# Kernel tuning notes

Hardware: AMD Instinct MI355X
Metric: run time of the kernel (lower is better)

## Reference

```python
import jax, jax.numpy as jnp
import numpy as np

B, N, D, C, H = 8, 2048, 768, 2048, 3072
ROPE_BASE = 10000.0


def rms_norm(x, scale, eps=1e-6):
    x32 = x.astype(jnp.float32)
    normed = x32 * jax.lax.rsqrt(jnp.mean(x32 * x32, axis=-1, keepdims=True) + eps)
    return normed.astype(x.dtype) * scale


def apply_rope(x, pos):
    # x: [..., T, D], pos: [..., T] int. Half-split (llama-style) rotary embedding.
    half = x.shape[-1] // 2
    inv_freq = 1.0 / (ROPE_BASE ** (jnp.arange(half, dtype=jnp.float32) / half))
    ang = pos.astype(jnp.float32)[..., None] * inv_freq  # [..., T, half]
    cos, sin = jnp.cos(ang), jnp.sin(ang)
    x1, x2 = x[..., :half], x[..., half:]
    return jnp.concatenate([x1 * cos - x2 * sin, x1 * sin + x2 * cos], axis=-1)


def setup_inputs() -> dict:
    key = jax.random.key(0)
    ks = jax.random.split(key, 12)
    inp = {
        "latents": jax.random.normal(ks[0], (B, N, D), dtype=jnp.float32),
        "tau": jnp.float32(1.0),
        "residual_scaling": jnp.float32(1.0),
        "gumbel_noise_scale": jnp.float32(0.5),
        "positions": jnp.sort(jax.random.randint(ks[1], (B, max(N, C)), 0, 2048), axis=-1),
        # learned parameters (torch Linear weights stored [out, in])
        "codebook": jax.random.normal(ks[2], (C, D), dtype=jnp.float32),
        "norm_context_scale": jnp.ones((D,), jnp.float32),
        "norm_queries_scale": jnp.ones((D,), jnp.float32),
        "norm_ff_scale": jnp.ones((D,), jnp.float32),
        "Wq": jax.random.normal(ks[3], (D, D), jnp.float32) / np.sqrt(D),
        "Wk": jax.random.normal(ks[4], (D, D), jnp.float32) / np.sqrt(D),
        "Wv": jax.random.normal(ks[5], (D, D), jnp.float32) / np.sqrt(D),
        "bv": jnp.zeros((D,), jnp.float32),
        "Wc": jax.random.normal(ks[6], (D, D), jnp.float32) / np.sqrt(D),
        "W1": jax.random.normal(ks[7], (H, D), jnp.float32) / np.sqrt(D),
        "W2": jax.random.normal(ks[8], (D, H), jnp.float32) / np.sqrt(H),
        "W3": jax.random.normal(ks[9], (H, D), jnp.float32) / np.sqrt(D),
    }
    return inp


def reference(latents, tau, residual_scaling, gumbel_noise_scale, positions,
              codebook, norm_context_scale, norm_queries_scale, norm_ff_scale,
              Wq, Wk, Wv, bv, Wc, W1, W2, W3):
    scale = jnp.sqrt(jnp.float32(D))
    normed_context = rms_norm(codebook, norm_context_scale)        # [C, D]
    normed_queries = rms_norm(latents, norm_queries_scale)         # [B, N, D]

    q = jnp.einsum('bnd,ed->bne', normed_queries, Wq)              # [B, N, D]
    k = normed_context @ Wk.T                                      # [C, D]
    v = normed_context @ Wv.T + bv                                 # [C, D]

    q = apply_rope(q, positions[:, :N])                            # [B, N, D]
    k = apply_rope(jnp.broadcast_to(k, (B, C, D)), positions[:, :C])  # [B, C, D]

    log_alpha = jnp.einsum('bnd,bcd->bnc', q, k) / scale           # [B, N, C]

    u = jax.random.uniform(jax.random.key(42), log_alpha.shape, dtype=jnp.float32)
    gumbel = -jnp.log(-jnp.log(u + 1e-10) + 1e-10)
    log_alpha_tau = (log_alpha + gumbel_noise_scale * gumbel) / tau
    z = jax.nn.softmax(log_alpha_tau, axis=-1)                     # [B, N, C]

    attn = jnp.einsum('bnc,cd->bnd', z, v)                         # [B, N, D]
    y = jnp.einsum('bnd,ed->bne', attn, Wc)
    attn_output = residual_scaling * latents + y

    h = rms_norm(attn_output, norm_ff_scale)
    ff = jnp.einsum('bnh,dh->bnd', jax.nn.silu(jnp.einsum('bnd,hd->bnh', h, W1)) * jnp.einsum('bnd,hd->bnh', h, W3), W2)
    codebook_output = attn_output + ff
    return (codebook_output, log_alpha, log_alpha_tau, z)
```

## Files before the change

kernel.cpp:

```cpp
#include <hip/hip_runtime.h>
#include <cstdint>
#include <cstddef>


typedef __bf16 bf16_t;
typedef __bf16 bf16x8 __attribute__((ext_vector_type(8)));
typedef float  f32x4  __attribute__((ext_vector_type(4)));
typedef float  f32x16 __attribute__((ext_vector_type(16)));

#define B_    8
#define N_    2048
#define D_    768
#define C_    2048
#define H_    3072
#define NROWS 16384

#define WQ_OFF 0
#define WK_OFF 589824
#define WV_OFF 1179648
#define WC_OFF 1769472
#define W1_OFF 2359296
#define W3_OFF 4718592
#define W2_OFF 7077888
#define WTOT   9437184

#define WS_W     0ull
#define WS_TRIG  18874368ull
#define WS_VCT   25165824ull
#define WS_NC    28311552ull
#define WS_NQ    31457280ull
#define WS_Z     56623104ull
#define WS_H     28311552ull
#define WS_G     157286400ull
#define WS_VB    257949696ull

#define DO_CB    0ull
#define DO_LA    50331648ull
#define DO_LAT   184549376ull
#define DO_Z     318767104ull
#define DO_QBASE 184549376ull
#define DO_KBASE (184549376ull + 50331648ull)
#define DO_QROPE (234881024ull + 6291456ull)
#define DO_KROPE (241172480ull + 25165824ull)

__device__ __forceinline__ void gl_lds16(const void* g, void* l) {
  __builtin_amdgcn_global_load_lds((__attribute__((address_space(1))) void*)(g),
                                   (__attribute__((address_space(3))) void*)(l),
                                   16, 0, 0);
}

__device__ __forceinline__ void block_sync() {
  __builtin_amdgcn_sched_barrier(0);
  asm volatile("" ::: "memory");
  __builtin_amdgcn_s_barrier();
  asm volatile("" ::: "memory");
  __builtin_amdgcn_sched_barrier(0);
}

__device__ __forceinline__ uint32_t rotl32(uint32_t v, int d) {
  return (v << d) | (v >> (32 - d));
}
__device__ __forceinline__ void tf_round(uint32_t& x0, uint32_t& x1, int r) {
  x0 += x1; x1 = rotl32(x1, r); x1 ^= x0;
}
__device__ __forceinline__ uint2 threefry2x32(uint32_t k0, uint32_t k1,
                                              uint32_t x0, uint32_t x1) {
  const uint32_t k2 = k0 ^ k1 ^ 0x1BD11BDAu;
  x0 += k0; x1 += k1;
  tf_round(x0,x1,13); tf_round(x0,x1,15); tf_round(x0,x1,26); tf_round(x0,x1,6);
  x0 += k1; x1 += k2 + 1u;
  tf_round(x0,x1,17); tf_round(x0,x1,29); tf_round(x0,x1,16); tf_round(x0,x1,24);
  x0 += k2; x1 += k0 + 2u;
  tf_round(x0,x1,13); tf_round(x0,x1,15); tf_round(x0,x1,26); tf_round(x0,x1,6);
  x0 += k0; x1 += k1 + 3u;
  tf_round(x0,x1,17); tf_round(x0,x1,29); tf_round(x0,x1,16); tf_round(x0,x1,24);
  x0 += k1; x1 += k2 + 4u;
  tf_round(x0,x1,13); tf_round(x0,x1,15); tf_round(x0,x1,26); tf_round(x0,x1,6);
  x0 += k2; x1 += k0 + 5u;
  return make_uint2(x0, x1);
}

#define SWZ(o) ((o) ^ ((((o) >> 7) & 3) << 4))

#define PHASE_MFMA_OPEN() do { \
    block_sync(); \
    asm volatile("s_waitcnt lgkmcnt(0)" ::: "memory"); \
    __builtin_amdgcn_sched_barrier(0); \
    __builtin_amdgcn_s_setprio(1); \
  } while (0)
#define PHASE_MFMA_CLOSE() do { \
    __builtin_amdgcn_s_setprio(0); \
    __builtin_amdgcn_sched_barrier(0); \
  } while (0)

#define ROWMAP32(rg, kg) (((rg) & 3) + 8 * ((rg) >> 2) + 4 * (kg))

template <int EPI>
__global__ __launch_bounds__(512, 2) void gemm8p(
    const bf16_t* __restrict__ A, const bf16_t* __restrict__ B,
    void* outp, const void* auxp, const float* sptr,
    int M, int N, int K, long sA, long sB, long sO)
{
  __shared__ bf16_t As[2][2][8192];
  __shared__ bf16_t Bs[2][2][8192];
  const int tid  = threadIdx.x;
  const int lane = tid & 63;
  const int wid  = tid >> 6;
  const int wm = wid >> 2, wn = wid & 3;
  const int l31 = lane & 31, kg = lane >> 5;

  const int lin = (blockIdx.z * gridDim.y + blockIdx.y) * gridDim.x + blockIdx.x;
  const int swzb = (lin & 7) * 64 + (lin >> 3);
  const int bz = swzb >> 6;
  const int ny = (swzb & 63) >> 3;
  const int nx = swzb & 7;

  const bf16_t* Ab = A + (size_t)bz * (size_t)sA;
  const bf16_t* Bb = B + (size_t)bz * (size_t)sB;
  const int tm = ny * 256;
  const int tn = nx * 256;
  const int nt = K >> 6;

  const bf16_t *srcA0, *srcA1, *srcB0, *srcB1;
  {
    const int d0 = wid * 1024 + lane * 16;
    const int p0 = SWZ(d0);
    srcA0 = Ab + (size_t)(tm + (p0 >> 6)) * K + ((p0 & 63) >> 1);
    srcB0 = Bb + (size_t)(tn + (p0 >> 6)) * K + ((p0 & 63) >> 1);
    const int d1 = 8192 + wid * 1024 + lane * 16;
    const int p1 = SWZ(d1);
    srcA1 = Ab + (size_t)(tm + (p1 >> 6)) * K + ((p1 & 63) >> 1);
    srcB1 = Bb + (size_t)(tn + (p1 >> 6)) * K + ((p1 & 63) >> 1);
  }
  bf16_t* dstA = &As[0][0][0] + wid * 512;
  bf16_t* dstB = &Bs[0][0][0] + wid * 512;

  int olA[4][2], olB[2][2];
  #pragma unroll
  for (int mb = 0; mb < 4; ++mb)
    #pragma unroll
    for (int u = 0; u < 2; ++u) {
      const int o = ((wm * 128 + mb * 32 + l31) << 6) + u * 32 + (kg << 4);
      olA[mb][u] = SWZ(o);
    }
  #pragma unroll
  for (int nb = 0; nb < 2; ++nb)
    #pragma unroll
    for (int u = 0; u < 2; ++u) {
      const int o = ((wn * 64 + nb * 32 + l31) << 6) + u * 32 + (kg << 4);
      olB[nb][u] = SWZ(o);
    }

#define STG_A(tile_, kk_) do { \
    const size_t ko_ = (size_t)(tile_) * 64 + (size_t)(kk_) * 32; \
    bf16_t* db_ = dstA + (((tile_) & 1) ? 16384 : 0) + ((kk_) ? 8192 : 0); \
    gl_lds16(srcA0 + ko_, db_); \
    gl_lds16(srcA1 + ko_, db_ + 4096); \
  } while (0)
#define STG_B(tile_, kk_) do { \
    const size_t ko_ = (size_t)(tile_) * 64 + (size_t)(kk_) * 32; \
    bf16_t* db_ = dstB + (((tile_) & 1) ? 16384 : 0) + ((kk_) ? 8192 : 0); \
    gl_lds16(srcB0 + ko_, db_); \
    gl_lds16(srcB1 + ko_, db_ + 4096); \
  } while (0)

  f32x16 acc[4][2] = {};

  STG_A(0, 0); STG_B(0, 0); STG_A(0, 1); STG_B(0, 1);
  STG_B(1, 0); STG_A(1, 0); STG_B(1, 1);
  asm volatile("s_waitcnt vmcnt(6)" ::: "memory");
  block_sync();

  for (int t = 0; t < nt; ++t) {
    const int s = t & 1;
    bf16x8 bfr[2][2];
    #pragma unroll
    for (int q = 0; q < 4; ++q) {
      const int kk = q >> 1, mh = q & 1;
      if (q == 0)      { if (t + 1 < nt) STG_A(t + 1, 1); }
      else if (q == 1) { if (t + 2 < nt) STG_B(t + 2, 0); }
      else if (q == 2) { if (t + 2 < nt) STG_A(t + 2, 0); }
      else             { if (t + 2 < nt) STG_B(t + 2, 1); }
      if (mh == 0) {
        const char* Bbase = (const char*)&Bs[s][kk][0];
        #pragma unroll
        for (int nb = 0; nb < 2; ++nb)
          #pragma unroll
          for (int u = 0; u < 2; ++u)
            bfr[nb][u] = *(const bf16x8*)(Bbase + olB[nb][u]);
      }
      const char* Abase = (const char*)&As[s][kk][0];
      bf16x8 af[2][2];
      #pragma unroll
      for (int j = 0; j < 2; ++j)
        #pragma unroll
        for (int u = 0; u < 2; ++u)
          af[j][u] = *(const bf16x8*)(Abase + olA[mh * 2 + j][u]);
      PHASE_MFMA_OPEN();
      #pragma unroll
      for (int u = 0; u < 2; ++u)
        #pragma unroll
        for (int j = 0; j < 2; ++j)
          #pragma unroll
          for (int nb = 0; nb < 2; ++nb)
            acc[mh * 2 + j][nb] =
              __builtin_amdgcn_mfma_f32_32x32x16_bf16(af[j][u], bfr[nb][u], acc[mh * 2 + j][nb], 0, 0, 0);
      PHASE_MFMA_CLOSE();
      if (q == 3) asm volatile("s_waitcnt vmcnt(6)" ::: "memory");
      block_sync();
    }
  }
#undef STG_A
#undef STG_B

  #pragma unroll
  for (int mb = 0; mb < 4; ++mb) {
    #pragma unroll
    for (int nb = 0; nb < 2; ++nb) {
      const int cg = tn + wn * 64 + nb * 32 + l31;
      #pragma unroll
      for (int rg = 0; rg < 16; ++rg) {
        const int r = tm + wm * 128 + mb * 32 + ROWMAP32(rg, kg);
        const float v = acc[mb][nb][rg];
        const size_t idx = (size_t)r * N + cg;
        if (EPI == 1) {
          ((float*)outp)[(size_t)bz * sO + idx] = v * 0.03608439182435161f;
        } else {
          ((float*)outp)[(size_t)bz * sO + idx] = v;
        }
      }
    }
  }
}

template <int EPI>
__global__ __launch_bounds__(512, 2) void gemm_n384(
    const bf16_t* __restrict__ A, const bf16_t* __restrict__ B,
    void* outp, const void* auxp, const float* sptr, int K)
{
  __shared__ bf16_t As[2][2][4096];
  __shared__ bf16_t Bs[2][2][12288];
  const int tid  = threadIdx.x;
  const int lane = tid & 63;
  const int wid  = tid >> 6;
  const int wm = wid >> 2, wn = wid & 3;
  const int l31 = lane & 31, kg = lane >> 5;

  const int lin = blockIdx.y * 2 + blockIdx.x;
  const int swzb = (lin & 7) * 32 + (lin >> 3);
  const int ny = swzb >> 1;
  const int nx = swzb & 1;

  const int tm = ny * 128;
  const int tn = nx * 384;
  const int nt = K >> 6;

  const bf16_t *srcA, *srcB0, *srcB1, *srcB2;
  {
    const int d = wid * 1024 + lane * 16;
    const int p = SWZ(d);
    srcA = A + (size_t)(tm + (p >> 6)) * K + ((p & 63) >> 1);
    srcB0 = B + (size_t)(tn + (p >> 6)) * K + ((p & 63) >> 1);
    const int d1 = 8192 + d, p1 = SWZ(d1);
    srcB1 = B + (size_t)(tn + (p1 >> 6)) * K + ((p1 & 63) >> 1);
    const int d2 = 16384 + d, p2 = SWZ(d2);
    srcB2 = B + (size_t)(tn + (p2 >> 6)) * K + ((p2 & 63) >> 1);
  }
  bf16_t* dstA = &As[0][0][0] + wid * 512;
  bf16_t* dstB = &Bs[0][0][0] + wid * 512;

  int olA[2][2], olB[3][2];
  #pragma unroll
  for (int mb = 0; mb < 2; ++mb)
    #pragma unroll
    for (int u = 0; u < 2; ++u) {
      const int o = ((wm * 64 + mb * 32 + l31) << 6) + u * 32 + (kg << 4);
      olA[mb][u] = SWZ(o);
    }
  #pragma unroll
  for (int nb = 0; nb < 3; ++nb)
    #pragma unroll
    for (int u = 0; u < 2; ++u) {
      const int o = ((wn * 96 + nb * 32 + l31) << 6) + u * 32 + (kg << 4);
      olB[nb][u] = SWZ(o);
    }

#define STG_A(tile_, kk_) do { \
    const size_t ko_ = (size_t)(tile_) * 64 + (size_t)(kk_) * 32; \
    gl_lds16(srcA + ko_, dstA + (((tile_) & 1) ? 8192 : 0) + ((kk_) ? 4096 : 0)); \
  } while (0)
#define STG_B(tile_, kk_) do { \
    const size_t ko_ = (size_t)(tile_) * 64 + (size_t)(kk_) * 32; \
    bf16_t* db_ = dstB + (((tile_) & 1) ? 24576 : 0) + ((kk_) ? 12288 : 0); \
    gl_lds16(srcB0 + ko_, db_); \
    gl_lds16(srcB1 + ko_, db_ + 4096); \
    gl_lds16(srcB2 + ko_, db_ + 8192); \
  } while (0)

  f32x16 acc[2][3] = {};

  STG_A(0, 0); STG_B(0, 0); STG_A(0, 1); STG_B(0, 1);
  STG_B(1, 0); STG_A(1, 0); STG_B(1, 1);
  asm volatile("s_waitcnt vmcnt(7)" ::: "memory");
  block_sync();

  for (int t = 0; t < nt; ++t) {
    const int s = t & 1;
    bf16x8 bfr[3][2];
    #pragma unroll
    for (int q = 0; q < 4; ++q) {
      const int kk = q >> 1, mh = q & 1;
      if (q == 0)      { if (t + 1 < nt) STG_A(t + 1, 1); }
      else if (q == 1) { if (t + 2 < nt) STG_B(t + 2, 0); }
      else if (q == 2) { if (t + 2 < nt) STG_A(t + 2, 0); }
      else             { if (t + 2 < nt) STG_B(t + 2, 1); }
      if (mh == 0) {
        const char* Bbase = (const char*)&Bs[s][kk][0];
        #pragma unroll
        for (int nb = 0; nb < 3; ++nb)
          #pragma unroll
          for (int u = 0; u < 2; ++u)
            bfr[nb][u] = *(const bf16x8*)(Bbase + olB[nb][u]);
      }
      const char* Abase = (const char*)&As[s][kk][0];
      bf16x8 af[2];
      #pragma unroll
      for (int u = 0; u < 2; ++u)
        af[u] = *(const bf16x8*)(Abase + olA[mh][u]);
      PHASE_MFMA_OPEN();
      #pragma unroll
      for (int u = 0; u < 2; ++u)
        #pragma unroll
        for (int nb = 0; nb < 3; ++nb)
          acc[mh][nb] =
            __builtin_amdgcn_mfma_f32_32x32x16_bf16(af[u], bfr[nb][u], acc[mh][nb], 0, 0, 0);
      PHASE_MFMA_CLOSE();
      if (q == 3) asm volatile("s_waitcnt vmcnt(7)" ::: "memory");
      block_sync();
    }
  }
#undef STG_A
#undef STG_B

  const float sval = (EPI == 5) ? sptr[0] : 0.0f;
  #pragma unroll
  for (int mb = 0; mb < 2; ++mb) {
    #pragma unroll
    for (int nb = 0; nb < 3; ++nb) {
      const int cg = tn + wn * 96 + nb * 32 + l31;
      #pragma unroll
      for (int rg = 0; rg < 16; ++rg) {
        const int r = tm + wm * 64 + mb * 32 + ROWMAP32(rg, kg);
        const float v = acc[mb][nb][rg];
        const size_t idx = (size_t)r * 768 + cg;
        if (EPI == 2) {
          ((bf16_t*)outp)[idx] = (bf16_t)v;
        } else if (EPI == 5) {
          ((float*)outp)[idx] = sval * ((const float*)auxp)[idx] + v;
        } else {
          ((float*)outp)[idx] = ((const float*)auxp)[idx] + v;
        }
      }
    }
  }
}

__global__ __launch_bounds__(512, 2) void gemm_ff13(
    const bf16_t* __restrict__ A, const bf16_t* __restrict__ B1,
    const bf16_t* __restrict__ B3, bf16_t* __restrict__ G, int K)
{
  __shared__ bf16_t As[2][2][8192];
  __shared__ bf16_t B1s[2][2][4096];
  __shared__ bf16_t B3s[2][2][4096];
  const int tid  = threadIdx.x;
  const int lane = tid & 63;
  const int wid  = tid >> 6;
  const int wm = wid >> 2, wn = wid & 3;
  const int l31 = lane & 31, kg = lane >> 5;
  const int xj = blockIdx.x & 7;
  const int bl = blockIdx.x >> 3;
  const int nt = K >> 6;

  const int d0 = wid * 1024 + lane * 16;
  const int p0 = SWZ(d0);
  const int a0r = p0 >> 6, a0c = (p0 & 63) >> 1;
  const int d1 = 8192 + d0;
  const int p1 = SWZ(d1);
  const int a1r = p1 >> 6, a1c = (p1 & 63) >> 1;

  bf16_t* dstA  = &As[0][0][0]  + wid * 512;
  bf16_t* dstB1 = &B1s[0][0][0] + wid * 512;
  bf16_t* dstB3 = &B3s[0][0][0] + wid * 512;

  int olA[4][2], olB[2];
  #pragma unroll
  for (int mb = 0; mb < 4; ++mb)
    #pragma unroll
    for (int u = 0; u < 2; ++u) {
      const int o = ((wm * 128 + mb * 32 + l31) << 6) + u * 32 + (kg << 4);
      olA[mb][u] = SWZ(o);
    }
  #pragma unroll
  for (int u = 0; u < 2; ++u) {
    const int o = ((wn * 32 + l31) << 6) + u * 32 + (kg << 4);
    olB[u] = SWZ(o);
  }

  int tm, tn;
  const bf16_t *srcA0, *srcA1, *srcB1p, *srcB3p;
#define SET_TILE(s_) do { \
    const int nx_ = xj * 3 + ((s_) % 3); \
    const int ny_ = bl * 2 + ((s_) / 3); \
    tm = ny_ * 256; tn = nx_ * 128; \
    srcA0  = A  + (size_t)(tm + a0r) * K + a0c; \
    srcA1  = A  + (size_t)(tm + a1r) * K + a1c; \
    srcB1p = B1 + (size_t)(tn + a0r) * K + a0c; \
    srcB3p = B3 + (size_t)(tn + a0r) * K + a0c; \
  } while (0)

#define STG_A(tile_, kk_) do { \
    const size_t ko_ = (size_t)(tile_) * 64 + (size_t)(kk_) * 32; \
    bf16_t* db_ = dstA + (((tile_) & 1) ? 16384 : 0) + ((kk_) ? 8192 : 0); \
    gl_lds16(srcA0 + ko_, db_); \
    gl_lds16(srcA1 + ko_, db_ + 4096); \
  } while (0)
#define STG_B(tile_, kk_) do { \
    const size_t ko_ = (size_t)(tile_) * 64 + (size_t)(kk_) * 32; \
    const int ro_ = (((tile_) & 1) ? 8192 : 0) + ((kk_) ? 4096 : 0); \
    gl_lds16(srcB1p + ko_, dstB1 + ro_); \
    gl_lds16(srcB3p + ko_, dstB3 + ro_); \
  } while (0)
#define PROLOGUE() do { \
    STG_A(0, 0); STG_B(0, 0); STG_A(0, 1); STG_B(0, 1); \
    STG_B(1, 0); STG_A(1, 0); STG_B(1, 1); \
  } while (0)

  SET_TILE(0);
  PROLOGUE();
  asm volatile("s_waitcnt vmcnt(6)" ::: "memory");
  block_sync();

  for (int sidx = 0; sidx < 6; ++sidx) {
    f32x16 acc1[4] = {};
    f32x16 acc3[4] = {};

    for (int t = 0; t < nt; ++t) {
      const int s = t & 1;
      bf16x8 b1r[2], b3r[2];
      #pragma unroll
      for (int q = 0; q < 4; ++q) {
        const int kk = q >> 1, mh = q & 1;
        if (q == 0)      { if (t + 1 < nt) STG_A(t + 1, 1); }
        else if (q == 1) { if (t + 2 < nt) STG_B(t + 2, 0); }
        else if (q == 2) { if (t + 2 < nt) STG_A(t + 2, 0); }
        else             { if (t + 2 < nt) STG_B(t + 2, 1); }
        if (mh == 0) {
          const char* B1base = (const char*)&B1s[s][kk][0];
          const char* B3base = (const char*)&B3s[s][kk][0];
          #pragma unroll
          for (int u = 0; u < 2; ++u) {
            b1r[u] = *(const bf16x8*)(B1base + olB[u]);
            b3r[u] = *(const bf16x8*)(B3base + olB[u]);
          }
        }
        const char* Abase = (const char*)&As[s][kk][0];
        bf16x8 af[2][2];
        #pragma unroll
        for (int j = 0; j < 2; ++j)
          #pragma unroll
          for (int u = 0; u < 2; ++u)
            af[j][u] = *(const bf16x8*)(Abase + olA[mh * 2 + j][u]);
        PHASE_MFMA_OPEN();
        #pragma unroll
        for (int u = 0; u < 2; ++u)
          #pragma unroll
          for (int j = 0; j < 2; ++j) {
            acc1[mh * 2 + j] =
              __builtin_amdgcn_mfma_f32_32x32x16_bf16(af[j][u], b1r[u], acc1[mh * 2 + j], 0, 0, 0);
            acc3[mh * 2 + j] =
              __builtin_amdgcn_mfma_f32_32x32x16_bf16(af[j][u], b3r[u], acc3[mh * 2 + j], 0, 0, 0);
          }
        PHASE_MFMA_CLOSE();
        if (q == 3) asm volatile("s_waitcnt vmcnt(6)" ::: "memory");
        block_sync();
      }
    }

    const int cm = tm, cn = tn;
    if (sidx < 5) { SET_TILE(sidx + 1); PROLOGUE(); }

    #pragma unroll
    for (int mb = 0; mb < 4; ++mb) {
      const int cg = cn + wn * 32 + l31;
      #pragma unroll
      for (int rg = 0; rg < 16; ++rg) {
        const int r2 = cm + wm * 128 + mb * 32 + ROWMAP32(rg, kg);
        const float f1 = acc1[mb][rg];
        const float f3 = acc3[mb][rg];
        const float sg = f1 / (1.0f + __expf(-f1));
        G[(size_t)r2 * 3072 + cg] = (bf16_t)(sg * f3);
      }
    }

    if (sidx < 5) {
      asm volatile("s_waitcnt vmcnt(6)" ::: "memory");
      block_sync();
    }
  }
#undef STG_A
#undef STG_B
#undef PROLOGUE
#undef SET_TILE
}

__global__ __launch_bounds__(256) void gemm_kv(
    const bf16_t* __restrict__ A, const bf16_t* __restrict__ Bk,
    const bf16_t* __restrict__ Bv, bf16_t* __restrict__ kout,
    bf16_t* __restrict__ vout, const float* __restrict__ bias,
    int M, int N, int K)
{
  __shared__ bf16_t Asl[128 * 64];
  __shared__ bf16_t Bks[128 * 64];
  __shared__ bf16_t Bvs[128 * 64];
  const int tid  = threadIdx.x;
  const int lane = tid & 63;
  const int wid  = tid >> 6;
  const int tm = blockIdx.y * 128;
  const int tn = blockIdx.x * 128;
  const int row0 = (wid & 1) * 64;
  const int col0 = (wid >> 1) * 64;
  const int fr = lane & 15;
  const int fg = lane >> 4;

  f32x4 acck[4][4] = {};
  f32x4 accv[4][4] = {};

  for (int k0 = 0; k0 < K; k0 += 64) {
    #pragma unroll
    for (int i = 0; i < 4; ++i) {
      const int ebase = (i * 4 + wid) * 512;
      const int e0 = ebase + lane * 8;
      const int r  = e0 >> 6;
      const int c  = e0 & 63;
      gl_lds16(A  + (size_t)(tm + r) * K + (k0 + c), &Asl[ebase]);
      gl_lds16(Bk + (size_t)(tn + r) * K + (k0 + c), &Bks[ebase]);
      gl_lds16(Bv + (size_t)(tn + r) * K + (k0 + c), &Bvs[ebase]);
    }
    __syncthreads();

    #pragma unroll
    for (int kk = 0; kk < 2; ++kk) {
      bf16x8 af[4], bk[4], bv2[4];
      #pragma unroll
      for (int m = 0; m < 4; ++m)
        af[m] = *(const bf16x8*)&Asl[(row0 + m * 16 + fr) * 64 + kk * 32 + fg * 8];
      #pragma unroll
      for (int n = 0; n < 4; ++n) {
        bk[n]  = *(const bf16x8*)&Bks[(col0 + n * 16 + fr) * 64 + kk * 32 + fg * 8];
        bv2[n] = *(const bf16x8*)&Bvs[(col0 + n * 16 + fr) * 64 + kk * 32 + fg * 8];
      }
      #pragma unroll
      for (int m = 0; m < 4; ++m) {
        #pragma unroll
        for (int n = 0; n < 4; ++n) {
          acck[m][n] = __builtin_amdgcn_mfma_f32_16x16x32_bf16(af[m], bk[n],  acck[m][n], 0, 0, 0);
          accv[m][n] = __builtin_amdgcn_mfma_f32_16x16x32_bf16(af[m], bv2[n], accv[m][n], 0, 0, 0);
        }
      }
    }
    __syncthreads();
  }

  #pragma unroll
  for (int m = 0; m < 4; ++m) {
    const int rb = row0 + m * 16 + fg * 4;
    #pragma unroll
    for (int n = 0; n < 4; ++n) {
      const int cg = tn + col0 + n * 16 + fr;
      #pragma unroll
      for (int j = 0; j < 4; ++j) {
        const int r = tm + rb + j;
        kout[(size_t)r * N + cg] = (bf16_t)acck[m][n][j];
        vout[(size_t)r * N + cg] = (bf16_t)(accv[m][n][j] + bias[cg]);
      }
    }
  }
}

template <int EPI>
__global__ __launch_bounds__(256) void gemm_bt(
    const bf16_t* __restrict__ A, const bf16_t* __restrict__ B,
    void* outp, const void* auxp, int M, int N, int K)
{
  __shared__ bf16_t Asl[128 * 64];
  __shared__ bf16_t Bsl[128 * 64];
  const int tid  = threadIdx.x;
  const int lane = tid & 63;
  const int wid  = tid >> 6;
  const int tm = blockIdx.y * 128;
  const int tn = blockIdx.x * 128;
  const int row0 = (wid & 1) * 64;
  const int col0 = (wid >> 1) * 64;
  const int fr = lane & 15;
  const int fg = lane >> 4;

  f32x4 acc[4][4] = {};

  for (int k0 = 0; k0 < K; k0 += 64) {
    #pragma unroll
    for (int i = 0; i < 4; ++i) {
      const int ebase = (i * 4 + wid) * 512;
      const int e0 = ebase + lane * 8;
      const int r  = e0 >> 6;
      const int c  = e0 & 63;
      gl_lds16(A + (size_t)(tm + r) * K + (k0 + c), &Asl[ebase]);
      gl_lds16(B + (size_t)(tn + r) * K + (k0 + c), &Bsl[ebase]);
    }
    __syncthreads();

    #pragma unroll
    for (int kk = 0; kk < 2; ++kk) {
      bf16x8 af[4], bfv[4];
      #pragma unroll
      for (int m = 0; m < 4; ++m)
        af[m] = *(const bf16x8*)&Asl[(row0 + m * 16 + fr) * 64 + kk * 32 + fg * 8];
      #pragma unroll
      for (int n = 0; n < 4; ++n)
        bfv[n] = *(const bf16x8*)&Bsl[(col0 + n * 16 + fr) * 64 + kk * 32 + fg * 8];
      #pragma unroll
      for (int m = 0; m < 4; ++m) {
        #pragma unroll
        for (int n = 0; n < 4; ++n)
          acc[m][n] = __builtin_amdgcn_mfma_f32_16x16x32_bf16(af[m], bfv[n], acc[m][n], 0, 0, 0);
      }
    }
    __syncthreads();
  }

  #pragma unroll
  for (int m = 0; m < 4; ++m) {
    const int rb = row0 + m * 16 + fg * 4;
    #pragma unroll
    for (int n = 0; n < 4; ++n) {
      const int cg = tn + col0 + n * 16 + fr;
      #pragma unroll
      for (int j = 0; j < 4; ++j) {
        const int r = tm + rb + j;
        const float v = acc[m][n][j];
        if (EPI == 7) {
          ((bf16_t*)outp)[(size_t)cg * M + r] = (bf16_t)v;
        } else {
          ((bf16_t*)outp)[(size_t)r * N + cg] = (bf16_t)v;
        }
      }
    }
  }
}

__global__ __launch_bounds__(256) void rms_all(
    const float* __restrict__ cb, const float* __restrict__ lt,
    const float* __restrict__ ncs, const float* __restrict__ nqs,
    bf16_t* __restrict__ nc, bf16_t* __restrict__ nq)
{
  const int row = blockIdx.x, t = threadIdx.x;
  const float* xr;
  const float* scale;
  bf16_t* orow;
  if (row < 2048) {
    xr = cb + (size_t)row * 768; scale = ncs; orow = nc + (size_t)row * 768;
  } else {
    const int r2 = row - 2048;
    xr = lt + (size_t)r2 * 768; scale = nqs; orow = nq + (size_t)r2 * 768;
  }
  const float v0 = xr[t], v1 = xr[t + 256], v2 = xr[t + 512];
  float ss = v0 * v0 + v1 * v1 + v2 * v2;
  #pragma unroll
  for (int m = 32; m; m >>= 1) ss += __shfl_xor(ss, m);
  __shared__ float red[4];
  if ((t & 63) == 0) red[t >> 6] = ss;
  __syncthreads();
  const float tot = red[0] + red[1] + red[2] + red[3];
  const float inv = rsqrtf(tot / 768.0f + 1e-6f);
  orow[t]       = (bf16_t)(v0 * inv * scale[t]);
  orow[t + 256] = (bf16_t)(v1 * inv * scale[t + 256]);
  orow[t + 512] = (bf16_t)(v2 * inv * scale[t + 512]);
}

__global__ __launch_bounds__(256) void rms_rows(const float* __restrict__ x,
                                                const float* __restrict__ scale,
                                                bf16_t* __restrict__ out)
{
  const int row = blockIdx.x, t = threadIdx.x;
  const float* xr = x + (size_t)row * 768;
  const float v0 = xr[t], v1 = xr[t + 256], v2 = xr[t + 512];
  float ss = v0 * v0 + v1 * v1 + v2 * v2;
  #pragma unroll
  for (int m = 32; m; m >>= 1) ss += __shfl_xor(ss, m);
  __shared__ float red[4];
  if ((t & 63) == 0) red[t >> 6] = ss;
  __syncthreads();
  const float tot = red[0] + red[1] + red[2] + red[3];
  const float inv = rsqrtf(tot / 768.0f + 1e-6f);
  bf16_t* orow = out + (size_t)row * 768;
  orow[t]       = (bf16_t)(v0 * inv * scale[t]);
  orow[t + 256] = (bf16_t)(v1 * inv * scale[t + 256]);
  orow[t + 512] = (bf16_t)(v2 * inv * scale[t + 512]);
}

__global__ __launch_bounds__(128) void trig_fill(float* __restrict__ trig)
{
  const int p = blockIdx.x, t = threadIdx.x;
  #pragma unroll
  for (int j = 0; j < 3; ++j) {
    const int i = t + j * 128;
    const float invf = expf(-(float)i * (9.210340371976184f / 384.0f));
    const float ang  = (float)p * invf;
    trig[(size_t)p * 768 + i]       = cosf(ang);
    trig[(size_t)p * 768 + 384 + i] = sinf(ang);
  }
}

__global__ __launch_bounds__(128) void rope_qk(const bf16_t* __restrict__ qsrc,
                                               const bf16_t* __restrict__ ksrc,
                                               const int* __restrict__ pos,
                                               const float* __restrict__ trig,
                                               bf16_t* __restrict__ qdst,
                                               bf16_t* __restrict__ kdst)
{
  const int bid = blockIdx.x, t = threadIdx.x;
  const bf16_t* s;
  bf16_t* d;
  int p;
  if (bid < NROWS) {
    p = pos[bid];
    s = qsrc + (size_t)bid * 768;
    d = qdst + (size_t)bid * 768;
  } else {
    const int row = bid - NROWS;
    p = pos[row];
    s = ksrc + (size_t)(row & 2047) * 768;
    d = kdst + (size_t)row * 768;
  }
  const float* tr = trig + (size_t)p * 768;
  #pragma unroll
  for (int j = 0; j < 3; ++j) {
    const int i = t + j * 128;
    const float x1 = (float)s[i], x2 = (float)s[i + 384];
    const float c = tr[i], sn = tr[i + 384];
    d[i]       = (bf16_t)(x1 * c - x2 * sn);
    d[i + 384] = (bf16_t)(x1 * sn + x2 * c);
  }
}

__global__ __launch_bounds__(256) void softmax_g(const float* __restrict__ la,
                                                 float* __restrict__ lat,
                                                 float* __restrict__ z,
                                                 bf16_t* __restrict__ zb,
                                                 const float* __restrict__ taup,
                                                 const float* __restrict__ gnsp)
{
  const int row = blockIdx.x, t = threadIdx.x;
  const float tau = taup[0], gns = gnsp[0];
  const float* lar = la + (size_t)row * 2048;
  float* latr = lat + (size_t)row * 2048;
  float* zr   = z   + (size_t)row * 2048;
  bf16_t* zbr = zb  + (size_t)row * 2048;
  const uint32_t base = (uint32_t)row * 2048u;

  float vals[8];
  float mx = -3.0e38f;
  #pragma unroll
  for (int j = 0; j < 8; ++j) {
    const int c = t + j * 256;
    const uint32_t flat = base + (uint32_t)c;
    const uint2 rr = threefry2x32(0u, 42u, 0u, flat);
    const uint32_t bits = rr.x ^ rr.y;
    const float u = __uint_as_float((bits >> 9) | 0x3f800000u) - 1.0f;
    const float gum = -__logf(-__logf(u + 1e-10f) + 1e-10f);
    const float v = (lar[c] + gns * gum) / tau;
    vals[j] = v;
    latr[c] = v;
    mx = fmaxf(mx, v);
  }
  #pragma unroll
  for (int m = 32; m; m >>= 1) mx = fmaxf(mx, __shfl_xor(mx, m));
  __shared__ float redm[4];
  if ((t & 63) == 0) redm[t >> 6] = mx;
  __syncthreads();
  mx = fmaxf(fmaxf(redm[0], redm[1]), fmaxf(redm[2], redm[3]));

  float sum = 0.0f;
  #pragma unroll
  for (int j = 0; j < 8; ++j) { vals[j] = __expf(vals[j] - mx); sum += vals[j]; }
  #pragma unroll
  for (int m = 32; m; m >>= 1) sum += __shfl_xor(sum, m);
  __shared__ float reds[4];
  if ((t & 63) == 0) reds[t >> 6] = sum;
  __syncthreads();
  sum = reds[0] + reds[1] + reds[2] + reds[3];

  const float rinv = 1.0f / sum;
  #pragma unroll
  for (int j = 0; j < 8; ++j) {
    const int c = t + j * 256;
    const float zz = vals[j] * rinv;
    zr[c]  = zz;
    zbr[c] = (bf16_t)zz;
  }
}

__global__ __launch_bounds__(256) void convert_w(
    const float* __restrict__ wq, const float* __restrict__ wk,
    const float* __restrict__ wv, const float* __restrict__ wc,
    const float* __restrict__ w1, const float* __restrict__ w3,
    const float* __restrict__ w2, bf16_t* __restrict__ dst)
{
  const int idx = blockIdx.x * 256 + threadIdx.x;
  const float* src; int off;
  if      (idx < 589824)  { src = wq; off = 0; }
  else if (idx < 1179648) { src = wk; off = 589824; }
  else if (idx < 1769472) { src = wv; off = 1179648; }
  else if (idx < 2359296) { src = wc; off = 1769472; }
  else if (idx < 4718592) { src = w1; off = 2359296; }
  else if (idx < 7077888) { src = w3; off = 4718592; }
  else                    { src = w2; off = 7077888; }
  dst[idx] = (bf16_t)src[idx - off];
}

extern "C" void kernel_launch(void* const* d_in, const int* in_sizes, int n_in,
                              void* d_out, int out_size, void* d_ws, size_t ws_size,
                              hipStream_t stream)
{
  (void)in_sizes; (void)n_in; (void)out_size; (void)ws_size;
  const float* latents   = (const float*)d_in[0];
  const float* taup      = (const float*)d_in[1];
  const float* rsp       = (const float*)d_in[2];
  const float* gnsp      = (const float*)d_in[3];
  const int*   positions = (const int*)d_in[4];
  const float* codebook  = (const float*)d_in[5];
  const float* ncs       = (const float*)d_in[6];
  const float* nqs       = (const float*)d_in[7];
  const float* nfs       = (const float*)d_in[8];
  const float* Wq = (const float*)d_in[9];
  const float* Wk = (const float*)d_in[10];
  const float* Wv = (const float*)d_in[11];
  const float* bv = (const float*)d_in[12];
  const float* Wc = (const float*)d_in[13];
  const float* W1 = (const float*)d_in[14];
  const float* W2 = (const float*)d_in[15];
  const float* W3 = (const float*)d_in[16];

  char* ws = (char*)d_ws;
  char* ob = (char*)d_out;

  bf16_t* wbf  = (bf16_t*)(ws + WS_W);
  float*  trig = (float*)(ws + WS_TRIG);
  bf16_t* vcT  = (bf16_t*)(ws + WS_VCT);
  bf16_t* nc   = (bf16_t*)(ws + WS_NC);
  bf16_t* nq   = (bf16_t*)(ws + WS_NQ);
  bf16_t* zbuf = (bf16_t*)(ws + WS_Z);
  bf16_t* hbuf = (bf16_t*)(ws + WS_H);
  bf16_t* gbuf = (bf16_t*)(ws + WS_G);
  bf16_t* vbuf = (bf16_t*)(ws + WS_VB);

  float*  out_cb  = (float*)(ob + DO_CB);
  float*  out_la  = (float*)(ob + DO_LA);
  float*  out_lat = (float*)(ob + DO_LAT);
  float*  out_z   = (float*)(ob + DO_Z);
  bf16_t* qbase   = (bf16_t*)(ob + DO_QBASE);
  bf16_t* kbase   = (bf16_t*)(ob + DO_KBASE);
  bf16_t* qrope   = (bf16_t*)(ob + DO_QROPE);
  bf16_t* krope   = (bf16_t*)(ob + DO_KROPE);

  convert_w<<<dim3(WTOT / 256), dim3(256), 0, stream>>>(Wq, Wk, Wv, Wc, W1, W3, W2, wbf);
  rms_all<<<dim3(C_ + NROWS), dim3(256), 0, stream>>>(codebook, latents, ncs, nqs, nc, nq);
  trig_fill<<<dim3(2048), dim3(128), 0, stream>>>(trig);

  gemm_kv<<<dim3(6, 16), dim3(256), 0, stream>>>(nc, wbf + WK_OFF, wbf + WV_OFF,
                                                 kbase, vbuf, bv, C_, D_, D_);
  gemm_bt<7><<<dim3(6, 16), dim3(256), 0, stream>>>(vbuf, wbf + WC_OFF, vcT, nullptr, C_, D_, D_);
  gemm_n384<2><<<dim3(2, 128), dim3(512), 0, stream>>>(nq, wbf + WQ_OFF, qbase, nullptr, nullptr, D_);

  rope_qk<<<dim3(2 * NROWS), dim3(128), 0, stream>>>(qbase, kbase, positions, trig, qrope, krope);

  gemm8p<1><<<dim3(8, 8, 8), dim3(512), 0, stream>>>(qrope, krope, out_la, nullptr, nullptr,
                                                     N_, C_, D_, (long)N_ * D_, (long)C_ * D_, (long)N_ * C_);

  softmax_g<<<dim3(NROWS), dim3(256), 0, stream>>>(out_la, out_lat, out_z, zbuf, taup, gnsp);

  gemm_n384<5><<<dim3(2, 128), dim3(512), 0, stream>>>(zbuf, vcT, out_cb, latents, rsp, C_);

  rms_rows<<<dim3(NROWS), dim3(256), 0, stream>>>(out_cb, nfs, hbuf);

  gemm_ff13<<<dim3(256), dim3(512), 0, stream>>>(hbuf, wbf + W1_OFF, wbf + W3_OFF, gbuf, D_);
  gemm_n384<6><<<dim3(2, 128), dim3(512), 0, stream>>>(gbuf, wbf + W2_OFF, out_cb, out_cb, nullptr, H_);
}
```

Baseline: 846.1 us.

## Halve pipeline phases per k-tile and remap persistent FFN tile order

Restructures the main GEMM loops in three kernels from four phases per k-tile to two. Each phase now loads all A and B fragments and issues the full MFMA set, which halves the block barriers, and the vmcnt waits are adjusted to match the new staging order, with a full drain near the end of the loop. The fused W1/W3 kernel also changes its persistent tile order so that each block sweeps six consecutive N tiles of the same M rows, aiming for better A reuse in L2. The trade-off is higher register pressure from holding more fragments at once and less fine-grained overlap of loads with MFMAs.

New measurement: 904.5 us. +6.9%, slower.

```diff
diff --git a/kernel.cpp b/kernel.cpp
--- a/kernel.cpp
+++ b/kernel.cpp
@@ -93,6 +93,11 @@
     __builtin_amdgcn_sched_barrier(0); \
   } while (0)
 
+#define PHASE_WAIT(t_, nt_) do { \
+    if ((t_) + 2 < (nt_)) asm volatile("s_waitcnt vmcnt(8)" ::: "memory"); \
+    else                  asm volatile("s_waitcnt vmcnt(0)" ::: "memory"); \
+  } while (0)
+
 #define ROWMAP32(rg, kg) (((rg) & 3) + 8 * ((rg) >> 2) + 4 * (kg))
 
 template <int EPI>
@@ -166,47 +171,43 @@
 
   f32x16 acc[4][2] = {};
 
-  STG_A(0, 0); STG_B(0, 0); STG_A(0, 1); STG_B(0, 1);
-  STG_B(1, 0); STG_A(1, 0); STG_B(1, 1);
-  asm volatile("s_waitcnt vmcnt(6)" ::: "memory");
+  STG_A(0, 0); STG_B(0, 0); STG_A(0, 1); STG_B(0, 1); STG_A(1, 0); STG_B(1, 0);
+  asm volatile("s_waitcnt vmcnt(8)" ::: "memory");
   block_sync();
 
   for (int t = 0; t < nt; ++t) {
     const int s = t & 1;
-    bf16x8 bfr[2][2];
-    #pragma unroll
-    for (int q = 0; q < 4; ++q) {
-      const int kk = q >> 1, mh = q & 1;
-      if (q == 0)      { if (t + 1 < nt) STG_A(t + 1, 1); }
-      else if (q == 1) { if (t + 2 < nt) STG_B(t + 2, 0); }
-      else if (q == 2) { if (t + 2 < nt) STG_A(t + 2, 0); }
-      else             { if (t + 2 < nt) STG_B(t + 2, 1); }
-      if (mh == 0) {
-        const char* Bbase = (const char*)&Bs[s][kk][0];
-        #pragma unroll
-        for (int nb = 0; nb < 2; ++nb)
-          #pragma unroll
-          for (int u = 0; u < 2; ++u)
-            bfr[nb][u] = *(const bf16x8*)(Bbase + olB[nb][u]);
+    #pragma unroll
+    for (int kk = 0; kk < 2; ++kk) {
+      if (kk == 0) {
+        if (t + 1 < nt) { STG_A(t + 1, 1); STG_B(t + 1, 1); }
+      } else {
+        if (t + 2 < nt) { STG_A(t + 2, 0); STG_B(t + 2, 0); }
       }
       const char* Abase = (const char*)&As[s][kk][0];
-      bf16x8 af[2][2];
-      #pragma unroll
-      for (int j = 0; j < 2; ++j)
+      const char* Bbase = (const char*)&Bs[s][kk][0];
+      bf16x8 af[4][2], bfr[2][2];
+      #pragma unroll
+      for (int mb = 0; mb < 4; ++mb)
         #pragma unroll
         for (int u = 0; u < 2; ++u)
-          af[j][u] = *(const bf16x8*)(Abase + olA[mh * 2 + j][u]);
+          af[mb][u] = *(const bf16x8*)(Abase + olA[mb][u]);
+      #pragma unroll
+      for (int nb = 0; nb < 2; ++nb)
+        #pragma unroll
+        for (int u = 0; u < 2; ++u)
+          bfr[nb][u] = *(const bf16x8*)(Bbase + olB[nb][u]);
       PHASE_MFMA_OPEN();
       #pragma unroll
       for (int u = 0; u < 2; ++u)
         #pragma unroll
-        for (int j = 0; j < 2; ++j)
+        for (int mb = 0; mb < 4; ++mb)
           #pragma unroll
           for (int nb = 0; nb < 2; ++nb)
-            acc[mh * 2 + j][nb] =
-              __builtin_amdgcn_mfma_f32_32x32x16_bf16(af[j][u], bfr[nb][u], acc[mh * 2 + j][nb], 0, 0, 0);
+            acc[mb][nb] =
+              __builtin_amdgcn_mfma_f32_32x32x16_bf16(af[mb][u], bfr[nb][u], acc[mb][nb], 0, 0, 0);
       PHASE_MFMA_CLOSE();
-      if (q == 3) asm volatile("s_waitcnt vmcnt(6)" ::: "memory");
+      PHASE_WAIT(t, nt);
       block_sync();
     }
   }
@@ -299,43 +300,43 @@
 
   f32x16 acc[2][3] = {};
 
-  STG_A(0, 0); STG_B(0, 0); STG_A(0, 1); STG_B(0, 1);
-  STG_B(1, 0); STG_A(1, 0); STG_B(1, 1);
-  asm volatile("s_waitcnt vmcnt(7)" ::: "memory");
+  STG_A(0, 0); STG_B(0, 0); STG_A(0, 1); STG_B(0, 1); STG_A(1, 0); STG_B(1, 0);
+  asm volatile("s_waitcnt vmcnt(8)" ::: "memory");
   block_sync();
 
   for (int t = 0; t < nt; ++t) {
     const int s = t & 1;
-    bf16x8 bfr[3][2];
-    #pragma unroll
-    for (int q = 0; q < 4; ++q) {
-      const int kk = q >> 1, mh = q & 1;
-      if (q == 0)      { if (t + 1 < nt) STG_A(t + 1, 1); }
-      else if (q == 1) { if (t + 2 < nt) STG_B(t + 2, 0); }
-      else if (q == 2) { if (t + 2 < nt) STG_A(t + 2, 0); }
-      else             { if (t + 2 < nt) STG_B(t + 2, 1); }
-      if (mh == 0) {
-        const char* Bbase = (const char*)&Bs[s][kk][0];
-        #pragma unroll
-        for (int nb = 0; nb < 3; ++nb)
+    #pragma unroll
+    for (int kk = 0; kk < 2; ++kk) {
+      if (kk == 0) {
+        if (t + 1 < nt) { STG_A(t + 1, 1); STG_B(t + 1, 1); }
+      } else {
+        if (t + 2 < nt) { STG_A(t + 2, 0); STG_B(t + 2, 0); }
+      }
+      const char* Abase = (const char*)&As[s][kk][0];
+      const char* Bbase = (const char*)&Bs[s][kk][0];
+      bf16x8 af[2][2], bfr[3][2];
+      #pragma unroll
+      for (int mb = 0; mb < 2; ++mb)
+        #pragma unroll
+        for (int u = 0; u < 2; ++u)
+          af[mb][u] = *(const bf16x8*)(Abase + olA[mb][u]);
+      #pragma unroll
+      for (int nb = 0; nb < 3; ++nb)
+        #pragma unroll
+        for (int u = 0; u < 2; ++u)
+          bfr[nb][u] = *(const bf16x8*)(Bbase + olB[nb][u]);
+      PHASE_MFMA_OPEN();
+      #pragma unroll
+      for (int u = 0; u < 2; ++u)
+        #pragma unroll
+        for (int mb = 0; mb < 2; ++mb)
           #pragma unroll
-          for (int u = 0; u < 2; ++u)
-            bfr[nb][u] = *(const bf16x8*)(Bbase + olB[nb][u]);
-      }
-      const char* Abase = (const char*)&As[s][kk][0];
-      bf16x8 af[2];
-      #pragma unroll
-      for (int u = 0; u < 2; ++u)
-        af[u] = *(const bf16x8*)(Abase + olA[mh][u]);
-      PHASE_MFMA_OPEN();
-      #pragma unroll
-      for (int u = 0; u < 2; ++u)
-        #pragma unroll
-        for (int nb = 0; nb < 3; ++nb)
-          acc[mh][nb] =
-            __builtin_amdgcn_mfma_f32_32x32x16_bf16(af[u], bfr[nb][u], acc[mh][nb], 0, 0, 0);
+          for (int nb = 0; nb < 3; ++nb)
+            acc[mb][nb] =
+              __builtin_amdgcn_mfma_f32_32x32x16_bf16(af[mb][u], bfr[nb][u], acc[mb][nb], 0, 0, 0);
       PHASE_MFMA_CLOSE();
-      if (q == 3) asm volatile("s_waitcnt vmcnt(7)" ::: "memory");
+      PHASE_WAIT(t, nt);
       block_sync();
     }
   }
@@ -409,8 +410,8 @@
   int tm, tn;
   const bf16_t *srcA0, *srcA1, *srcB1p, *srcB3p;
 #define SET_TILE(s_) do { \
-    const int nx_ = xj * 3 + ((s_) % 3); \
-    const int ny_ = bl * 2 + ((s_) / 3); \
+    const int ny_ = xj * 8 + (bl & 7); \
+    const int nx_ = (bl >> 3) * 6 + (s_); \
     tm = ny_ * 256; tn = nx_ * 128; \
     srcA0  = A  + (size_t)(tm + a0r) * K + a0c; \
     srcA1  = A  + (size_t)(tm + a1r) * K + a1c; \
@@ -431,13 +432,12 @@
     gl_lds16(srcB3p + ko_, dstB3 + ro_); \
   } while (0)
 #define PROLOGUE() do { \
-    STG_A(0, 0); STG_B(0, 0); STG_A(0, 1); STG_B(0, 1); \
-    STG_B(1, 0); STG_A(1, 0); STG_B(1, 1); \
+    STG_A(0, 0); STG_B(0, 0); STG_A(0, 1); STG_B(0, 1); STG_A(1, 0); STG_B(1, 0); \
   } while (0)
 
   SET_TILE(0);
   PROLOGUE();
-  asm volatile("s_waitcnt vmcnt(6)" ::: "memory");
+  asm volatile("s_waitcnt vmcnt(8)" ::: "memory");
   block_sync();
 
   for (int sidx = 0; sidx < 6; ++sidx) {
@@ -446,42 +446,39 @@
 
     for (int t = 0; t < nt; ++t) {
       const int s = t & 1;
-      bf16x8 b1r[2], b3r[2];
-      #pragma unroll
-      for (int q = 0; q < 4; ++q) {
-        const int kk = q >> 1, mh = q & 1;
-        if (q == 0)      { if (t + 1 < nt) STG_A(t + 1, 1); }
-        else if (q == 1) { if (t + 2 < nt) STG_B(t + 2, 0); }
-        else if (q == 2) { if (t + 2 < nt) STG_A(t + 2, 0); }
-        else             { if (t + 2 < nt) STG_B(t + 2, 1); }
-        if (mh == 0) {
-          const char* B1base = (const char*)&B1s[s][kk][0];
-          const char* B3base = (const char*)&B3s[s][kk][0];
-          #pragma unroll
-          for (int u = 0; u < 2; ++u) {
-            b1r[u] = *(const bf16x8*)(B1base + olB[u]);
-            b3r[u] = *(const bf16x8*)(B3base + olB[u]);
-          }
+      #pragma unroll
+      for (int kk = 0; kk < 2; ++kk) {
+        if (kk == 0) {
+          if (t + 1 < nt) { STG_A(t + 1, 1); STG_B(t + 1, 1); }
+        } else {
+          if (t + 2 < nt) { STG_A(t + 2, 0); STG_B(t + 2, 0); }
         }
-        const char* Abase = (const char*)&As[s][kk][0];
-        bf16x8 af[2][2];
-        #pragma unroll
-        for (int j = 0; j < 2; ++j)
+        const char* Abase  = (const char*)&As[s][kk][0];
+        const char* B1base = (const char*)&B1s[s][kk][0];
+        const char* B3base = (const char*)&B3s[s][kk][0];
+        bf16x8 af[4][2], b1r[2], b3r[2];
+        #pragma unroll
+        for (int mb = 0; mb < 4; ++mb)
           #pragma unroll
           for (int u = 0; u < 2; ++u)
-            af[j][u] = *(const bf16x8*)(Abase + olA[mh * 2 + j][u]);
+            af[mb][u] = *(const bf16x8*)(Abase + olA[mb][u]);
+        #pragma unroll
+        for (int u = 0; u < 2; ++u) {
+          b1r[u] = *(const bf16x8*)(B1base + olB[u]);
+          b3r[u] = *(const bf16x8*)(B3base + olB[u]);
+        }
         PHASE_MFMA_OPEN();
         #pragma unroll
         for (int u = 0; u < 2; ++u)
           #pragma unroll
-          for (int j = 0; j < 2; ++j) {
-            acc1[mh * 2 + j] =
-              __builtin_amdgcn_mfma_f32_32x32x16_bf16(af[j][u], b1r[u], acc1[mh * 2 + j], 0, 0, 0);
-            acc3[mh * 2 + j] =
-              __builtin_amdgcn_mfma_f32_32x32x16_bf16(af[j][u], b3r[u], acc3[mh * 2 + j], 0, 0, 0);
+          for (int mb = 0; mb < 4; ++mb) {
+            acc1[mb] =
+              __builtin_amdgcn_mfma_f32_32x32x16_bf16(af[mb][u], b1r[u], acc1[mb], 0, 0, 0);
+            acc3[mb] =
+              __builtin_amdgcn_mfma_f32_32x32x16_bf16(af[mb][u], b3r[u], acc3[mb], 0, 0, 0);
           }
         PHASE_MFMA_CLOSE();
-        if (q == 3) asm volatile("s_waitcnt vmcnt(6)" ::: "memory");
+        PHASE_WAIT(t, nt);
         block_sync();
       }
     }
@@ -503,7 +500,7 @@
     }
 
     if (sidx < 5) {
-      asm volatile("s_waitcnt vmcnt(6)" ::: "memory");
+      asm volatile("s_waitcnt vmcnt(8)" ::: "memory");
       block_sync();
     }
   }
```

## Replace persistent 256x128 FF13 kernel with simple 128x128 tiled grid kernel

Applied to the files above, without the earlier changes.

The fused W1/W3 SwiGLU GEMM moves from a persistent 256-block kernel, where each block walks six 256x128 tiles with a 64-deep K pipeline, to a plain 24x128 grid of 256-thread blocks. Each block computes one 128x128 tile with a 32-deep K step and double-buffered LDS. The new loop reads all fragments, then issues prefetch and MFMAs under raised wave priority. This trades the larger tile's data reuse and cross-tile prologue overlap for more blocks, smaller LDS use and simpler scheduling, which may improve occupancy and load balance but adds global traffic per FLOP.

New measurement: 910.7 us. 1.08x slower.

```diff
diff --git a/kernel.cpp b/kernel.cpp
--- a/kernel.cpp
+++ b/kernel.cpp
@@ -365,152 +365,115 @@
   }
 }
 
-__global__ __launch_bounds__(512, 2) void gemm_ff13(
+__global__ __launch_bounds__(256) void gemm_ff13L(
     const bf16_t* __restrict__ A, const bf16_t* __restrict__ B1,
     const bf16_t* __restrict__ B3, bf16_t* __restrict__ G, int K)
 {
-  __shared__ bf16_t As[2][2][8192];
-  __shared__ bf16_t B1s[2][2][4096];
-  __shared__ bf16_t B3s[2][2][4096];
+  __shared__ bf16_t As[2][4096];
+  __shared__ bf16_t B1s[2][4096];
+  __shared__ bf16_t B3s[2][4096];
   const int tid  = threadIdx.x;
   const int lane = tid & 63;
   const int wid  = tid >> 6;
-  const int wm = wid >> 2, wn = wid & 3;
   const int l31 = lane & 31, kg = lane >> 5;
-  const int xj = blockIdx.x & 7;
-  const int bl = blockIdx.x >> 3;
-  const int nt = K >> 6;
-
-  const int d0 = wid * 1024 + lane * 16;
-  const int p0 = SWZ(d0);
-  const int a0r = p0 >> 6, a0c = (p0 & 63) >> 1;
-  const int d1 = 8192 + d0;
-  const int p1 = SWZ(d1);
-  const int a1r = p1 >> 6, a1c = (p1 & 63) >> 1;
-
-  bf16_t* dstA  = &As[0][0][0]  + wid * 512;
-  bf16_t* dstB1 = &B1s[0][0][0] + wid * 512;
-  bf16_t* dstB3 = &B3s[0][0][0] + wid * 512;
-
-  int olA[4][2], olB[2];
-  #pragma unroll
-  for (int mb = 0; mb < 4; ++mb)
+  const int tm = blockIdx.y * 128;
+  const int tn = blockIdx.x * 128;
+  const int nt = K >> 5;
+
+  const bf16_t *srcA[2], *srcB1p[2], *srcB3p[2];
+  #pragma unroll
+  for (int i = 0; i < 2; ++i) {
+    const int d = i * 4096 + wid * 1024 + lane * 16;
+    const int p = SWZ(d);
+    const int r = p >> 6, c = (p & 63) >> 1;
+    srcA[i]   = A  + (size_t)(tm + r) * K + c;
+    srcB1p[i] = B1 + (size_t)(tn + r) * K + c;
+    srcB3p[i] = B3 + (size_t)(tn + r) * K + c;
+  }
+  bf16_t* dA  = &As[0][0]  + wid * 512;
+  bf16_t* dB1 = &B1s[0][0] + wid * 512;
+  bf16_t* dB3 = &B3s[0][0] + wid * 512;
+
+  int olA[2], olB[4][2];
+  #pragma unroll
+  for (int u = 0; u < 2; ++u) {
+    const int o = ((wid * 32 + l31) << 6) + u * 32 + (kg << 4);
+    olA[u] = SWZ(o);
+  }
+  #pragma unroll
+  for (int nb = 0; nb < 4; ++nb)
     #pragma unroll
     for (int u = 0; u < 2; ++u) {
-      const int o = ((wm * 128 + mb * 32 + l31) << 6) + u * 32 + (kg << 4);
-      olA[mb][u] = SWZ(o);
-    }
-  #pragma unroll
-  for (int u = 0; u < 2; ++u) {
-    const int o = ((wn * 32 + l31) << 6) + u * 32 + (kg << 4);
-    olB[u] = SWZ(o);
-  }
-
-  int tm, tn;
-  const bf16_t *srcA0, *srcA1, *srcB1p, *srcB3p;
-#define SET_TILE(s_) do { \
-    const int nx_ = xj * 3 + ((s_) % 3); \
-    const int ny_ = bl * 2 + ((s_) / 3); \
-    tm = ny_ * 256; tn = nx_ * 128; \
-    srcA0  = A  + (size_t)(tm + a0r) * K + a0c; \
-    srcA1  = A  + (size_t)(tm + a1r) * K + a1c; \
-    srcB1p = B1 + (size_t)(tn + a0r) * K + a0c; \
-    srcB3p = B3 + (size_t)(tn + a0r) * K + a0c; \
+      const int o = ((nb * 32 + l31) << 6) + u * 32 + (kg << 4);
+      olB[nb][u] = SWZ(o);
+    }
+
+#define STG(tile_) do { \
+    const size_t ko_ = (size_t)(tile_) * 32; \
+    const int so_ = ((tile_) & 1) ? 4096 : 0; \
+    gl_lds16(srcA[0]   + ko_, dA  + so_); \
+    gl_lds16(srcA[1]   + ko_, dA  + so_ + 2048); \
+    gl_lds16(srcB1p[0] + ko_, dB1 + so_); \
+    gl_lds16(srcB1p[1] + ko_, dB1 + so_ + 2048); \
+    gl_lds16(srcB3p[0] + ko_, dB3 + so_); \
+    gl_lds16(srcB3p[1] + ko_, dB3 + so_ + 2048); \
   } while (0)
 
-#define STG_A(tile_, kk_) do { \
-    const size_t ko_ = (size_t)(tile_) * 64 + (size_t)(kk_) * 32; \
-    bf16_t* db_ = dstA + (((tile_) & 1) ? 16384 : 0) + ((kk_) ? 8192 : 0); \
-    gl_lds16(srcA0 + ko_, db_); \
-    gl_lds16(srcA1 + ko_, db_ + 4096); \
-  } while (0)
-#define STG_B(tile_, kk_) do { \
-    const size_t ko_ = (size_t)(tile_) * 64 + (size_t)(kk_) * 32; \
-    const int ro_ = (((tile_) & 1) ? 8192 : 0) + ((kk_) ? 4096 : 0); \
-    gl_lds16(srcB1p + ko_, dstB1 + ro_); \
-    gl_lds16(srcB3p + ko_, dstB3 + ro_); \
-  } while (0)
-#define PROLOGUE() do { \
-    STG_A(0, 0); STG_B(0, 0); STG_A(0, 1); STG_B(0, 1); \
-    STG_B(1, 0); STG_A(1, 0); STG_B(1, 1); \
-  } while (0)
-
-  SET_TILE(0);
-  PROLOGUE();
+  f32x16 acc1[4] = {};
+  f32x16 acc3[4] = {};
+
+  STG(0); STG(1);
   asm volatile("s_waitcnt vmcnt(6)" ::: "memory");
   block_sync();
 
-  for (int sidx = 0; sidx < 6; ++sidx) {
-    f32x16 acc1[4] = {};
-    f32x16 acc3[4] = {};
-
-    for (int t = 0; t < nt; ++t) {
-      const int s = t & 1;
-      bf16x8 b1r[2], b3r[2];
-      #pragma unroll
-      for (int q = 0; q < 4; ++q) {
-        const int kk = q >> 1, mh = q & 1;
-        if (q == 0)      { if (t + 1 < nt) STG_A(t + 1, 1); }
-        else if (q == 1) { if (t + 2 < nt) STG_B(t + 2, 0); }
-        else if (q == 2) { if (t + 2 < nt) STG_A(t + 2, 0); }
-        else             { if (t + 2 < nt) STG_B(t + 2, 1); }
-        if (mh == 0) {
-          const char* B1base = (const char*)&B1s[s][kk][0];
-          const char* B3base = (const char*)&B3s[s][kk][0];
-          #pragma unroll
-          for (int u = 0; u < 2; ++u) {
-            b1r[u] = *(const bf16x8*)(B1base + olB[u]);
-            b3r[u] = *(const bf16x8*)(B3base + olB[u]);
-          }
-        }
-        const char* Abase = (const char*)&As[s][kk][0];
-        bf16x8 af[2][2];
-        #pragma unroll
-        for (int j = 0; j < 2; ++j)
-          #pragma unroll
-          for (int u = 0; u < 2; ++u)
-            af[j][u] = *(const bf16x8*)(Abase + olA[mh * 2 + j][u]);
-        PHASE_MFMA_OPEN();
-        #pragma unroll
-        for (int u = 0; u < 2; ++u)
-          #pragma unroll
-          for (int j = 0; j < 2; ++j) {
-            acc1[mh * 2 + j] =
-              __builtin_amdgcn_mfma_f32_32x32x16_bf16(af[j][u], b1r[u], acc1[mh * 2 + j], 0, 0, 0);
-            acc3[mh * 2 + j] =
-              __builtin_amdgcn_mfma_f32_32x32x16_bf16(af[j][u], b3r[u], acc3[mh * 2 + j], 0, 0, 0);
-          }
-        PHASE_MFMA_CLOSE();
-        if (q == 3) asm volatile("s_waitcnt vmcnt(6)" ::: "memory");
-        block_sync();
-      }
-    }
-
-    const int cm = tm, cn = tn;
-    if (sidx < 5) { SET_TILE(sidx + 1); PROLOGUE(); }
-
-    #pragma unroll
-    for (int mb = 0; mb < 4; ++mb) {
-      const int cg = cn + wn * 32 + l31;
-      #pragma unroll
-      for (int rg = 0; rg < 16; ++rg) {
-        const int r2 = cm + wm * 128 + mb * 32 + ROWMAP32(rg, kg);
-        const float f1 = acc1[mb][rg];
-        const float f3 = acc3[mb][rg];
-        const float sg = f1 / (1.0f + __expf(-f1));
-        G[(size_t)r2 * 3072 + cg] = (bf16_t)(sg * f3);
-      }
-    }
-
-    if (sidx < 5) {
-      asm volatile("s_waitcnt vmcnt(6)" ::: "memory");
-      block_sync();
-    }
-  }
-#undef STG_A
-#undef STG_B
-#undef PROLOGUE
-#undef SET_TILE
+  for (int t = 0; t < nt; ++t) {
+    const int s = t & 1;
+    const char* Abase  = (const char*)&As[s][0];
+    const char* B1base = (const char*)&B1s[s][0];
+    const char* B3base = (const char*)&B3s[s][0];
+    bf16x8 af[2], b1r[4][2], b3r[4][2];
+    #pragma unroll
+    for (int u = 0; u < 2; ++u)
+      af[u] = *(const bf16x8*)(Abase + olA[u]);
+    #pragma unroll
+    for (int nb = 0; nb < 4; ++nb)
+      #pragma unroll
+      for (int u = 0; u < 2; ++u) {
+        b1r[nb][u] = *(const bf16x8*)(B1base + olB[nb][u]);
+        b3r[nb][u] = *(const bf16x8*)(B3base + olB[nb][u]);
+      }
+    asm volatile("s_waitcnt lgkmcnt(0)" ::: "memory");
+    __builtin_amdgcn_sched_barrier(0);
+    block_sync();
+    if (t + 2 < nt) STG(t + 2);
+    __builtin_amdgcn_s_setprio(1);
+    #pragma unroll
+    for (int u = 0; u < 2; ++u)
+      #pragma unroll
+      for (int nb = 0; nb < 4; ++nb) {
+        acc1[nb] = __builtin_amdgcn_mfma_f32_32x32x16_bf16(af[u], b1r[nb][u], acc1[nb], 0, 0, 0);
+        acc3[nb] = __builtin_amdgcn_mfma_f32_32x32x16_bf16(af[u], b3r[nb][u], acc3[nb], 0, 0, 0);
+      }
+    __builtin_amdgcn_s_setprio(0);
+    __builtin_amdgcn_sched_barrier(0);
+    if (t + 2 < nt) asm volatile("s_waitcnt vmcnt(6)" ::: "memory");
+    else            asm volatile("s_waitcnt vmcnt(0)" ::: "memory");
+    block_sync();
+  }
+#undef STG
+
+  #pragma unroll
+  for (int nb = 0; nb < 4; ++nb) {
+    const int cg = tn + nb * 32 + l31;
+    #pragma unroll
+    for (int rg = 0; rg < 16; ++rg) {
+      const int r2 = tm + wid * 32 + ROWMAP32(rg, kg);
+      const float f1 = acc1[nb][rg];
+      const float f3 = acc3[nb][rg];
+      const float sg = f1 / (1.0f + __expf(-f1));
+      G[(size_t)r2 * 3072 + cg] = (bf16_t)(sg * f3);
+    }
+  }
 }
 
 __global__ __launch_bounds__(256) void gemm_kv(
@@ -892,6 +855,6 @@
 
   rms_rows<<<dim3(NROWS), dim3(256), 0, stream>>>(out_cb, nfs, hbuf);
 
-  gemm_ff13<<<dim3(256), dim3(512), 0, stream>>>(hbuf, wbf + W1_OFF, wbf + W3_OFF, gbuf, D_);
+  gemm_ff13L<<<dim3(24, 128), dim3(256), 0, stream>>>(hbuf, wbf + W1_OFF, wbf + W3_OFF, gbuf, D_);
   gemm_n384<6><<<dim3(2, 128), dim3(512), 0, stream>>>(gbuf, wbf + W2_OFF, out_cb, out_cb, nullptr, H_);
 }
```
